# Optimization experiments

Hardware: AMD Instinct MI355X
Metric: run time of the kernel (lower is better)

## Reference

```python
import jax, jax.numpy as jnp
import numpy as np

V_TH = 1.0  # IF neuron threshold (default v_threshold=1, v_reset=0)
SCALE = 1.0  # PoissonEncoder firing scale


def setup_inputs() -> dict:
    key = jax.random.key(0)
    k_x, k_n, k_w1, k_w2 = jax.random.split(key, 4)
    B, T, D_IN, D_H, D_OUT = 8192, 32, 784, 100, 10
    x = jax.random.uniform(k_x, (B, D_IN), dtype=jnp.float32)
    noise = jax.random.uniform(k_n, (T, B, D_IN), dtype=jnp.float32)
    W1 = jax.random.normal(k_w1, (D_H, D_IN), dtype=jnp.float32) * (1.0 / np.sqrt(D_IN))
    W2 = jax.random.normal(k_w2, (D_OUT, D_H), dtype=jnp.float32) * (1.0 / np.sqrt(D_H))
    return {"x": x, "noise": noise, "W1": W1, "W2": W2}


def reference(x, noise, W1, W2):
    # Poisson encoding: spike if uniform noise < scale * firing_rate.  [T,B,784]
    spikes = jnp.where(noise < SCALE * x[None, :, :], 1.0, 0.0).astype(x.dtype)

    B = x.shape[0]
    v0 = jnp.zeros((B, W1.shape[0]), dtype=x.dtype)          # membrane potential [B,100]
    logits0 = jnp.zeros((B, W2.shape[0]), dtype=x.dtype)      # accumulated logits [B,10]

    def step(carry, sp_t):
        v, logits = carry
        h = jnp.einsum('bi,hi->bh', sp_t, W1)                 # Linear 784->100 (no bias)
        v = v + h                                             # integrate
        spike = jnp.where(v - V_TH > 0, 1.0, 0.0).astype(h.dtype)  # fire
        v = v - spike * V_TH                                  # soft reset
        logits = logits + jnp.einsum('bh,oh->bo', spike, W2)  # Linear 100->10, accumulate
        return (v, logits), None

    (_, logits), _ = jax.lax.scan(step, (v0, logits0), spikes)
    return logits
```

## Files before the change

kernel.cpp:

```cpp
#include <hip/hip_runtime.h>
#include <hip/hip_bf16.h>
#include <cstdint>


typedef __attribute__((ext_vector_type(8))) short bf16x8;
typedef __attribute__((ext_vector_type(4))) float f32x4;

#define D_IN 784
#define NB 8192
#define KT 25
#define NTL 8

__device__ __forceinline__ void gload_lds16(const float* g, float* l) {
    __builtin_amdgcn_global_load_lds((const __attribute__((address_space(1))) void*)g,
                                     (__attribute__((address_space(3))) void*)l, 16, 0, 0);
}

__global__ void prep_w1(const float* __restrict__ W1, unsigned short* __restrict__ wf) {
    int idx = blockIdx.x * 256 + threadIdx.x;
    if (idx >= KT * NTL * 64) return;
    int l  = idx & 63;
    int nt = (idx >> 6) & 7;
    int kt = idx >> 9;
    int n  = nt * 16 + (l & 15);
    int i0 = kt * 32 + (l >> 4) * 8;
    size_t fbase = (size_t)(kt * 8 + nt) * 1024;
    #pragma unroll
    for (int j = 0; j < 8; ++j) {
        int i = i0 + j;
        float w = (n < 100 && i < D_IN) ? W1[n * D_IN + i] : 0.f;
        uint32_t ub = __float_as_uint(w);
        uint32_t rh = ub + 0x7FFFu + ((ub >> 16) & 1u);
        unsigned short h = (unsigned short)(rh >> 16);
        float hf = __uint_as_float(((uint32_t)h) << 16);
        float resid = w - hf;
        uint32_t ul = __float_as_uint(resid);
        uint32_t rl = ul + 0x7FFFu + ((ul >> 16) & 1u);
        unsigned short lo = (unsigned short)(rl >> 16);
        wf[fbase + l * 8 + j]       = h;
        wf[fbase + 512 + l * 8 + j] = lo;
    }
}

__global__ __launch_bounds__(256) void snn_gemm(const float* __restrict__ x,
                                                const float* __restrict__ noise,
                                                const unsigned short* __restrict__ wf,
                                                float* __restrict__ H) {
    __shared__ __align__(16) float sN[4096];
    __shared__ __align__(16) float sX[4096];
    const int tid   = threadIdx.x;
    const int lane  = tid & 63;
    const int wave  = tid >> 6;
    const int Mhalf = wave >> 1;
    const int Nhalf = wave & 1;
    const int M0    = blockIdx.x * 128;
    const int t     = M0 >> 13;
    const int b0    = M0 & (NB - 1);
    const float* nb = noise + (size_t)t * ((size_t)NB * D_IN);

    int sRow[4], sCg[4];
    #pragma unroll
    for (int i = 0; i < 4; ++i) {
        int s = i * 256 + tid;
        sRow[i] = s >> 3;
        sCg[i]  = (s & 7) ^ (sRow[i] & 7);
    }
    const int c0 = (lane >> 4) * 2;
    int fSlot[4][2];
    #pragma unroll
    for (int mt = 0; mt < 4; ++mt) {
        int row = Mhalf * 64 + mt * 16 + (lane & 15);
        fSlot[mt][0] = row * 8 + (c0 ^ (row & 7));
        fSlot[mt][1] = row * 8 + ((c0 + 1) ^ (row & 7));
    }

    f32x4 acc[4][4];
    #pragma unroll
    for (int i = 0; i < 4; ++i)
        #pragma unroll
        for (int j = 0; j < 4; ++j) acc[i][j] = (f32x4){0.f, 0.f, 0.f, 0.f};

    #pragma unroll 1
    for (int kt = 0; kt < KT; ++kt) {
        __syncthreads();
        #pragma unroll
        for (int i = 0; i < 4; ++i) {
            int colf = kt * 32 + sCg[i] * 4;
            if (kt == KT - 1 && sCg[i] >= 4) colf = (KT - 1) * 32;
            const size_t ro = (size_t)(b0 + sRow[i]) * D_IN + colf;
            const int base = i * 256 + wave * 64;
            gload_lds16(nb + ro, &sN[base * 4]);
            gload_lds16(x + ro,  &sX[base * 4]);
        }
        __syncthreads();

        bf16x8 afr[4];
        #pragma unroll
        for (int mt = 0; mt < 4; ++mt) {
            const float4 n0 = *reinterpret_cast<const float4*>(&sN[fSlot[mt][0] * 4]);
            const float4 n1 = *reinterpret_cast<const float4*>(&sN[fSlot[mt][1] * 4]);
            const float4 x0 = *reinterpret_cast<const float4*>(&sX[fSlot[mt][0] * 4]);
            const float4 x1 = *reinterpret_cast<const float4*>(&sX[fSlot[mt][1] * 4]);
            union { uint32_t u[4]; bf16x8 v; } pk;
            pk.u[0] = (n0.x < x0.x ? 0x3F80u : 0u) | (n0.y < x0.y ? 0x3F800000u : 0u);
            pk.u[1] = (n0.z < x0.z ? 0x3F80u : 0u) | (n0.w < x0.w ? 0x3F800000u : 0u);
            pk.u[2] = (n1.x < x1.x ? 0x3F80u : 0u) | (n1.y < x1.y ? 0x3F800000u : 0u);
            pk.u[3] = (n1.z < x1.z ? 0x3F80u : 0u) | (n1.w < x1.w ? 0x3F800000u : 0u);
            afr[mt] = pk.v;
        }
        #pragma unroll
        for (int nt = 0; nt < 4; ++nt) {
            const size_t fo = (size_t)(kt * 8 + Nhalf * 4 + nt) * 1024 + lane * 8;
            const bf16x8 bhi = *reinterpret_cast<const bf16x8*>(wf + fo);
            const bf16x8 blo = *reinterpret_cast<const bf16x8*>(wf + fo + 512);
            #pragma unroll
            for (int mt = 0; mt < 4; ++mt) {
                acc[mt][nt] = __builtin_amdgcn_mfma_f32_16x16x32_bf16(afr[mt], bhi, acc[mt][nt], 0, 0, 0);
                acc[mt][nt] = __builtin_amdgcn_mfma_f32_16x16x32_bf16(afr[mt], blo, acc[mt][nt], 0, 0, 0);
            }
        }
    }
    const int colBase   = Nhalf * 64 + (lane & 15);
    const int rowInTile = (lane >> 4) * 4;
    #pragma unroll
    for (int mt = 0; mt < 4; ++mt) {
        const size_t rg = (size_t)M0 + Mhalf * 64 + mt * 16 + rowInTile;
        #pragma unroll
        for (int nt = 0; nt < 4; ++nt) {
            const int col = colBase + nt * 16;
            #pragma unroll
            for (int r = 0; r < 4; ++r)
                H[(rg + r) * 128 + col] = acc[mt][nt][r];
        }
    }
}

__global__ __launch_bounds__(256) void snn_scan(const float* __restrict__ H,
                                                const float* __restrict__ W2,
                                                float* __restrict__ out) {
    __shared__ float cbuf[2][128];
    __shared__ float w2s[1000];
    const int tid = threadIdx.x;
    const int r = tid >> 7, h = tid & 127;
    const size_t b = (size_t)blockIdx.x * 2 + r;
    for (int i = tid; i < 1000; i += 256) w2s[i] = W2[i];

    float hv[32];
    #pragma unroll
    for (int t = 0; t < 32; ++t) hv[t] = H[((size_t)t * NB + b) * 128 + h];

    float v = 0.f, cnt = 0.f;
    #pragma unroll
    for (int t = 0; t < 32; ++t) {
        v += hv[t];
        float s = (v - 1.0f > 0.0f) ? 1.0f : 0.0f;
        v -= s;
        cnt += s;
    }
    cbuf[r][h] = cnt;
    __syncthreads();
    if (tid < 20) {
        const int rr = tid / 10, o = tid % 10;
        float s = 0.f;
        for (int hh = 0; hh < 100; ++hh) s += cbuf[rr][hh] * w2s[o * 100 + hh];
        out[((size_t)blockIdx.x * 2 + rr) * 10 + o] = s;
    }
}

extern "C" void kernel_launch(void* const* d_in, const int* in_sizes, int n_in,
                              void* d_out, int out_size, void* d_ws, size_t ws_size,
                              hipStream_t stream) {
    const float* x     = (const float*)d_in[0];
    const float* noise = (const float*)d_in[1];
    const float* W1    = (const float*)d_in[2];
    const float* W2    = (const float*)d_in[3];
    float* out = (float*)d_out;

    unsigned short* wf = (unsigned short*)d_ws;
    float* H = (float*)((char*)d_ws + (1u << 20));

    prep_w1<<<50, 256, 0, stream>>>(W1, wf);
    snn_gemm<<<2048, 256, 0, stream>>>(x, noise, wf, H);
    snn_scan<<<4096, 256, 0, stream>>>(H, W2, out);
}
```

Measured before the change: 360.7 us.

## Prefetch next K-tile to registers, store packed bf16 spikes in double-buffered LDS

```diff
diff --git a/kernel.cpp b/kernel.cpp
--- a/kernel.cpp
+++ b/kernel.cpp
@@ -10,11 +10,7 @@
 #define NB 8192
 #define KT 25
 #define NTL 8
-
-__device__ __forceinline__ void gload_lds16(const float* g, float* l) {
-    __builtin_amdgcn_global_load_lds((const __attribute__((address_space(1))) void*)g,
-                                     (__attribute__((address_space(3))) void*)l, 16, 0, 0);
-}
+#define DH 100
 
 __global__ void prep_w1(const float* __restrict__ W1, unsigned short* __restrict__ wf) {
     int idx = blockIdx.x * 256 + threadIdx.x;
@@ -28,7 +24,7 @@
     #pragma unroll
     for (int j = 0; j < 8; ++j) {
         int i = i0 + j;
-        float w = (n < 100 && i < D_IN) ? W1[n * D_IN + i] : 0.f;
+        float w = (n < DH && i < D_IN) ? W1[n * D_IN + i] : 0.f;
         uint32_t ub = __float_as_uint(w);
         uint32_t rh = ub + 0x7FFFu + ((ub >> 16) & 1u);
         unsigned short h = (unsigned short)(rh >> 16);
@@ -46,32 +42,34 @@
                                                 const float* __restrict__ noise,
                                                 const unsigned short* __restrict__ wf,
                                                 float* __restrict__ H) {
-    __shared__ __align__(16) float sN[4096];
-    __shared__ __align__(16) float sX[4096];
+    __shared__ __align__(16) unsigned short sS[2][4096];
     const int tid   = threadIdx.x;
     const int lane  = tid & 63;
     const int wave  = tid >> 6;
     const int Mhalf = wave >> 1;
     const int Nhalf = wave & 1;
-    const int M0    = blockIdx.x * 128;
-    const int t     = M0 >> 13;
-    const int b0    = M0 & (NB - 1);
+    const int L     = blockIdx.x;
+    const int btile = (L & 7) * 8 + ((L >> 3) & 7);
+    const int t     = L >> 6;
+    const int b0    = btile * 128;
     const float* nb = noise + (size_t)t * ((size_t)NB * D_IN);
 
-    int sRow[4], sCg[4];
+    int sRow[4], sGcol[4], wOff[4];
     #pragma unroll
     for (int i = 0; i < 4; ++i) {
-        int s = i * 256 + tid;
-        sRow[i] = s >> 3;
-        sCg[i]  = (s & 7) ^ (sRow[i] & 7);
-    }
-    const int c0 = (lane >> 4) * 2;
-    int fSlot[4][2];
+        int gg = i * 256 + tid;
+        sRow[i]  = gg >> 3;
+        sGcol[i] = gg & 7;
+        int g  = sGcol[i] >> 1;
+        int gp = g ^ ((sRow[i] >> 1) & 3);
+        wOff[i] = sRow[i] * 32 + gp * 8 + (sGcol[i] & 1) * 4;
+    }
+    int fOff[4];
     #pragma unroll
     for (int mt = 0; mt < 4; ++mt) {
         int row = Mhalf * 64 + mt * 16 + (lane & 15);
-        fSlot[mt][0] = row * 8 + (c0 ^ (row & 7));
-        fSlot[mt][1] = row * 8 + ((c0 + 1) ^ (row & 7));
+        int gp  = (lane >> 4) ^ ((row >> 1) & 3);
+        fOff[mt] = row * 32 + gp * 8;
     }
 
     f32x4 acc[4][4];
@@ -79,35 +77,41 @@
     for (int i = 0; i < 4; ++i)
         #pragma unroll
         for (int j = 0; j < 4; ++j) acc[i][j] = (f32x4){0.f, 0.f, 0.f, 0.f};
+
+    {
+        #pragma unroll
+        for (int i = 0; i < 4; ++i) {
+            const size_t ro = (size_t)(b0 + sRow[i]) * D_IN + sGcol[i] * 4;
+            const float4 nv = *reinterpret_cast<const float4*>(nb + ro);
+            const float4 xv = *reinterpret_cast<const float4*>(x + ro);
+            uint32_t u0 = (nv.x < xv.x ? 0x3F80u : 0u) | (nv.y < xv.y ? 0x3F800000u : 0u);
+            uint32_t u1 = (nv.z < xv.z ? 0x3F80u : 0u) | (nv.w < xv.w ? 0x3F800000u : 0u);
+            *reinterpret_cast<uint2*>(&sS[0][wOff[i]]) = make_uint2(u0, u1);
+        }
+        __syncthreads();
+    }
 
     #pragma unroll 1
     for (int kt = 0; kt < KT; ++kt) {
-        __syncthreads();
-        #pragma unroll
-        for (int i = 0; i < 4; ++i) {
-            int colf = kt * 32 + sCg[i] * 4;
-            if (kt == KT - 1 && sCg[i] >= 4) colf = (KT - 1) * 32;
-            const size_t ro = (size_t)(b0 + sRow[i]) * D_IN + colf;
-            const int base = i * 256 + wave * 64;
-            gload_lds16(nb + ro, &sN[base * 4]);
-            gload_lds16(x + ro,  &sX[base * 4]);
-        }
-        __syncthreads();
+        const unsigned short* rb = &sS[kt & 1][0];
+        unsigned short*       wb = &sS[(kt & 1) ^ 1][0];
+
+        float4 nr[4], xr[4];
+        if (kt < KT - 1) {
+            #pragma unroll
+            for (int i = 0; i < 4; ++i) {
+                int c = (kt + 1) * 32 + sGcol[i] * 4;
+                if (kt + 1 == KT - 1 && sGcol[i] >= 4) c = (KT - 1) * 32;
+                const size_t ro = (size_t)(b0 + sRow[i]) * D_IN + c;
+                nr[i] = *reinterpret_cast<const float4*>(nb + ro);
+                xr[i] = *reinterpret_cast<const float4*>(x + ro);
+            }
+        }
 
         bf16x8 afr[4];
         #pragma unroll
-        for (int mt = 0; mt < 4; ++mt) {
-            const float4 n0 = *reinterpret_cast<const float4*>(&sN[fSlot[mt][0] * 4]);
-            const float4 n1 = *reinterpret_cast<const float4*>(&sN[fSlot[mt][1] * 4]);
-            const float4 x0 = *reinterpret_cast<const float4*>(&sX[fSlot[mt][0] * 4]);
-            const float4 x1 = *reinterpret_cast<const float4*>(&sX[fSlot[mt][1] * 4]);
-            union { uint32_t u[4]; bf16x8 v; } pk;
-            pk.u[0] = (n0.x < x0.x ? 0x3F80u : 0u) | (n0.y < x0.y ? 0x3F800000u : 0u);
-            pk.u[1] = (n0.z < x0.z ? 0x3F80u : 0u) | (n0.w < x0.w ? 0x3F800000u : 0u);
-            pk.u[2] = (n1.x < x1.x ? 0x3F80u : 0u) | (n1.y < x1.y ? 0x3F800000u : 0u);
-            pk.u[3] = (n1.z < x1.z ? 0x3F80u : 0u) | (n1.w < x1.w ? 0x3F800000u : 0u);
-            afr[mt] = pk.v;
-        }
+        for (int mt = 0; mt < 4; ++mt)
+            afr[mt] = *reinterpret_cast<const bf16x8*>(rb + fOff[mt]);
         #pragma unroll
         for (int nt = 0; nt < 4; ++nt) {
             const size_t fo = (size_t)(kt * 8 + Nhalf * 4 + nt) * 1024 + lane * 8;
@@ -119,18 +123,31 @@
                 acc[mt][nt] = __builtin_amdgcn_mfma_f32_16x16x32_bf16(afr[mt], blo, acc[mt][nt], 0, 0, 0);
             }
         }
-    }
+
+        if (kt < KT - 1) {
+            #pragma unroll
+            for (int i = 0; i < 4; ++i) {
+                uint32_t u0 = (nr[i].x < xr[i].x ? 0x3F80u : 0u) | (nr[i].y < xr[i].y ? 0x3F800000u : 0u);
+                uint32_t u1 = (nr[i].z < xr[i].z ? 0x3F80u : 0u) | (nr[i].w < xr[i].w ? 0x3F800000u : 0u);
+                *reinterpret_cast<uint2*>(&wb[wOff[i]]) = make_uint2(u0, u1);
+            }
+        }
+        __syncthreads();
+    }
+
     const int colBase   = Nhalf * 64 + (lane & 15);
     const int rowInTile = (lane >> 4) * 4;
     #pragma unroll
     for (int mt = 0; mt < 4; ++mt) {
-        const size_t rg = (size_t)M0 + Mhalf * 64 + mt * 16 + rowInTile;
+        const size_t rg = (size_t)t * NB + b0 + Mhalf * 64 + mt * 16 + rowInTile;
         #pragma unroll
         for (int nt = 0; nt < 4; ++nt) {
             const int col = colBase + nt * 16;
-            #pragma unroll
-            for (int r = 0; r < 4; ++r)
-                H[(rg + r) * 128 + col] = acc[mt][nt][r];
+            if (col < DH) {
+                #pragma unroll
+                for (int r = 0; r < 4; ++r)
+                    H[(rg + r) * DH + col] = acc[mt][nt][r];
+            }
         }
     }
 }
@@ -138,31 +155,33 @@
 __global__ __launch_bounds__(256) void snn_scan(const float* __restrict__ H,
                                                 const float* __restrict__ W2,
                                                 float* __restrict__ out) {
-    __shared__ float cbuf[2][128];
+    __shared__ float cbuf[2][104];
     __shared__ float w2s[1000];
     const int tid = threadIdx.x;
     const int r = tid >> 7, h = tid & 127;
     const size_t b = (size_t)blockIdx.x * 2 + r;
     for (int i = tid; i < 1000; i += 256) w2s[i] = W2[i];
 
-    float hv[32];
-    #pragma unroll
-    for (int t = 0; t < 32; ++t) hv[t] = H[((size_t)t * NB + b) * 128 + h];
-
-    float v = 0.f, cnt = 0.f;
-    #pragma unroll
-    for (int t = 0; t < 32; ++t) {
-        v += hv[t];
-        float s = (v - 1.0f > 0.0f) ? 1.0f : 0.0f;
-        v -= s;
-        cnt += s;
-    }
-    cbuf[r][h] = cnt;
+    float cnt = 0.f;
+    if (h < DH) {
+        float hv[32];
+        #pragma unroll
+        for (int t = 0; t < 32; ++t) hv[t] = H[((size_t)t * NB + b) * DH + h];
+        float v = 0.f;
+        #pragma unroll
+        for (int t = 0; t < 32; ++t) {
+            v += hv[t];
+            float s = (v - 1.0f > 0.0f) ? 1.0f : 0.0f;
+            v -= s;
+            cnt += s;
+        }
+    }
+    if (h < DH) cbuf[r][h] = cnt;
     __syncthreads();
     if (tid < 20) {
         const int rr = tid / 10, o = tid % 10;
         float s = 0.f;
-        for (int hh = 0; hh < 100; ++hh) s += cbuf[rr][hh] * w2s[o * 100 + hh];
+        for (int hh = 0; hh < DH; ++hh) s += cbuf[rr][hh] * w2s[o * DH + hh];
         out[((size_t)blockIdx.x * 2 + rr) * 10 + o] = s;
     }
 }
```

Result: slower. 373.3 us (+3.5%).
